# Kernel optimization log

Hardware: AMD Instinct MI355X
Metric: run time of the kernel (lower is better)

## Reference

```python
import jax, jax.numpy as jnp
import numpy as np

N = 100000
E = 1600000
D = 64
ED = 16
L = 3


def setup_inputs() -> dict:
    key = jax.random.key(0)
    ks = jax.random.split(key, 12)
    s = 1.0 / np.sqrt(D)
    se = 1.0 / np.sqrt(ED)
    return {
        "x": jax.random.normal(ks[0], (N, D), dtype=jnp.float32),
        "edge_index": jax.random.randint(ks[1], (2, E), 0, N, dtype=jnp.int64),
        "edge_attr": jax.random.normal(ks[2], (E, ED), dtype=jnp.float32),
        "Wk": jax.random.normal(ks[3], (L, D, D), dtype=jnp.float32) * s,
        "bk": jnp.zeros((L, D), dtype=jnp.float32),
        "Wq": jax.random.normal(ks[4], (L, D, D), dtype=jnp.float32) * s,
        "bq": jnp.zeros((L, D), dtype=jnp.float32),
        "Wv": jax.random.normal(ks[5], (L, D, D), dtype=jnp.float32) * s,
        "bv": jnp.zeros((L, D), dtype=jnp.float32),
        "We": jax.random.normal(ks[6], (L, ED, D), dtype=jnp.float32) * se,
        "be": jnp.zeros((L, D), dtype=jnp.float32),
        "Wskip": jax.random.normal(ks[7], (L, D, D), dtype=jnp.float32) * s,
        "bias": jnp.zeros((L, D), dtype=jnp.float32),
        "Wl": jax.random.normal(ks[8], (D, 1), dtype=jnp.float32) * s,
        "bl": jnp.zeros((1,), dtype=jnp.float32),
    }


def _res_gated_conv(h, src, dst, edge_attr, Wk, bk, Wq, bq, Wv, bv, We, be, Wskip, bias):
    # PyG ResGatedGraphConv: eta = sigmoid(k_i + q_j + lin_edge(e)); out_i = sum_j eta * v_j + lin_skip(x_i) + bias
    k = h @ Wk + bk            # [N, D]
    q = h @ Wq + bq            # [N, D]
    v = h @ Wv + bv            # [N, D]
    e = edge_attr @ We + be    # [E, D]
    gate = jax.nn.sigmoid(k[dst] + q[src] + e)   # [E, D]
    msg = gate * v[src]                          # [E, D]
    agg = jax.ops.segment_sum(msg, dst, num_segments=N)  # scatter-add to targets
    return agg + h @ Wskip + bias


def reference(x, edge_index, edge_attr, Wk, bk, Wq, bq, Wv, bv, We, be, Wskip, bias, Wl, bl):
    src = edge_index[0]  # j (source, flow source_to_target)
    dst = edge_index[1]  # i (target)
    h = x
    h = jax.nn.elu(_res_gated_conv(h, src, dst, edge_attr, Wk[0], bk[0], Wq[0], bq[0], Wv[0], bv[0], We[0], be[0], Wskip[0], bias[0]))
    feat = jax.nn.elu(_res_gated_conv(h, src, dst, edge_attr, Wk[1], bk[1], Wq[1], bq[1], Wv[1], bv[1], We[1], be[1], Wskip[1], bias[1]))
    h = jax.nn.elu(_res_gated_conv(feat, src, dst, edge_attr, Wk[2], bk[2], Wq[2], bq[2], Wv[2], bv[2], We[2], be[2], Wskip[2], bias[2]))
    logits = h @ Wl + bl                         # [N, 1]
    return (jax.nn.sigmoid(logits), feat, jnp.concatenate((feat, logits), axis=1))
```

## Files before the change

### kernel.cpp

```cpp
#include <hip/hip_runtime.h>
#include <hip/hip_bf16.h>
#include <math.h>


#define D_CH 64
#define E_CH 16

__device__ __forceinline__ float bcastf(float v, int srclane) {
  return __int_as_float(__builtin_amdgcn_readlane(__float_as_int(v), srclane));
}

__global__ void k_detect(const unsigned int* __restrict__ ei, int* __restrict__ flag,
                         int n_samples) {
  __shared__ unsigned int red[256];
  unsigned int acc = 0;
  for (int i = threadIdx.x; i < n_samples; i += 256) acc |= ei[2 * i + 1];
  red[threadIdx.x] = acc;
  __syncthreads();
  for (int s = 128; s > 0; s >>= 1) {
    if (threadIdx.x < s) red[threadIdx.x] |= red[threadIdx.x + s];
    __syncthreads();
  }
  if (threadIdx.x == 0) flag[0] = (red[0] == 0u) ? 1 : 0;
}

__global__ void k_normalize(const void* __restrict__ ei, const int* __restrict__ flag,
                            int* __restrict__ src, int* __restrict__ dst, int E) {
  int e = blockIdx.x * blockDim.x + threadIdx.x;
  if (e >= E) return;
  if (flag[0]) {
    const long long* p = (const long long*)ei;
    src[e] = (int)p[e];
    dst[e] = (int)p[E + e];
  } else {
    const int* p = (const int*)ei;
    src[e] = p[e];
    dst[e] = p[E + e];
  }
}

__global__ void k_zero(int* __restrict__ p, int n) {
  int i = blockIdx.x * blockDim.x + threadIdx.x;
  if (i < n) p[i] = 0;
}

__global__ void k_hist(const int* __restrict__ dst, int* __restrict__ deg, int E) {
  int e = blockIdx.x * blockDim.x + threadIdx.x;
  if (e < E) atomicAdd(&deg[dst[e]], 1);
}

__global__ void k_scan(int* __restrict__ deg_cursor, int* __restrict__ offsets, int N) {
  __shared__ int buf[1024];
  __shared__ int carry;
  if (threadIdx.x == 0) carry = 0;
  __syncthreads();
  for (int base = 0; base < N; base += 1024) {
    int i = base + threadIdx.x;
    int val = (i < N) ? deg_cursor[i] : 0;
    buf[threadIdx.x] = val;
    __syncthreads();
    for (int off = 1; off < 1024; off <<= 1) {
      int t = (threadIdx.x >= off) ? buf[threadIdx.x - off] : 0;
      __syncthreads();
      buf[threadIdx.x] += t;
      __syncthreads();
    }
    int excl = buf[threadIdx.x] - val;
    int c = carry;
    int tot = buf[1023];
    __syncthreads();
    if (i < N) {
      offsets[i] = c + excl;
      deg_cursor[i] = c + excl;
    }
    if (threadIdx.x == 0) carry = c + tot;
    __syncthreads();
  }
  if (threadIdx.x == 0) offsets[N] = carry;
}

__global__ void k_scatter(const int* __restrict__ src, const int* __restrict__ dst,
                          int* __restrict__ cursor, int* __restrict__ csr_src,
                          int* __restrict__ csr_eid, int E) {
  int e = blockIdx.x * blockDim.x + threadIdx.x;
  if (e >= E) return;
  int d = dst[e];
  int p = atomicAdd(&cursor[d], 1);
  csr_src[p] = src[e];
  csr_eid[p] = e;
}

__global__ __launch_bounds__(256, 1) void k_nodelin(
    const float* __restrict__ hin, const float* __restrict__ Wa,
    const float* __restrict__ ba, const float* __restrict__ Wb,
    const float* __restrict__ bb, float* __restrict__ outa, float* __restrict__ outb,
    int N) {
  int lane = threadIdx.x & 63;
  int wave = blockIdx.x * (blockDim.x >> 6) + (threadIdx.x >> 6);
  int nwaves = gridDim.x * (blockDim.x >> 6);
  float wa[64], wb[64];
#pragma unroll
  for (int c = 0; c < 64; ++c) {
    wa[c] = Wa[c * 64 + lane];
    wb[c] = Wb[c * 64 + lane];
  }
  float bav = ba[lane], bbv = bb[lane];
  for (int i = wave; i < N; i += nwaves) {
    float h = hin[(size_t)i * 64 + lane];
    float a = bav, b = bbv;
#pragma unroll
    for (int c = 0; c < 64; ++c) {
      float hc = bcastf(h, c);
      a = fmaf(hc, wa[c], a);
      b = fmaf(hc, wb[c], b);
    }
    outa[(size_t)i * 64 + lane] = a;
    outb[(size_t)i * 64 + lane] = b;
  }
}

template <int MODE>
__global__ __launch_bounds__(256, 4) void k_edge(
    const int* __restrict__ offsets, const int* __restrict__ csr_src,
    const int* __restrict__ csr_eid, const float* __restrict__ kk,
    const float* __restrict__ qq, const float* __restrict__ vv,
    const float* __restrict__ base, const float* __restrict__ ea,
    const float* __restrict__ We, const float* __restrict__ be,
    float* __restrict__ hnext, float* __restrict__ dout,
    const float* __restrict__ Wl, const float* __restrict__ bl, int N) {
  int lane = threadIdx.x & 63;
  int wave = blockIdx.x * (blockDim.x >> 6) + (threadIdx.x >> 6);
  int nwaves = gridDim.x * (blockDim.x >> 6);
  float we[16];
#pragma unroll
  for (int c = 0; c < 16; ++c) we[c] = We[c * 64 + lane];
  float bev = be[lane];
  float wl = (MODE == 2) ? Wl[lane] : 0.f;
  float bl0 = (MODE == 2) ? bl[0] : 0.f;
  for (int i = wave; i < N; i += nwaves) {
    float ki = kk[(size_t)i * 64 + lane] + bev;
    float acc = base[(size_t)i * 64 + lane];
    int p0 = __builtin_amdgcn_readfirstlane(offsets[i]);
    int p1 = __builtin_amdgcn_readfirstlane(offsets[i + 1]);
    for (int p = p0; p < p1; ++p) {
      int j = __builtin_amdgcn_readfirstlane(csr_src[p]);
      int eid = __builtin_amdgcn_readfirstlane(csr_eid[p]);
      const float4* eaq = (const float4*)(ea + (size_t)eid * E_CH);
      float4 e0 = eaq[0], e1 = eaq[1], e2 = eaq[2], e3 = eaq[3];
      float ev = 0.f;
      ev = fmaf(e0.x, we[0], ev);  ev = fmaf(e0.y, we[1], ev);
      ev = fmaf(e0.z, we[2], ev);  ev = fmaf(e0.w, we[3], ev);
      ev = fmaf(e1.x, we[4], ev);  ev = fmaf(e1.y, we[5], ev);
      ev = fmaf(e1.z, we[6], ev);  ev = fmaf(e1.w, we[7], ev);
      ev = fmaf(e2.x, we[8], ev);  ev = fmaf(e2.y, we[9], ev);
      ev = fmaf(e2.z, we[10], ev); ev = fmaf(e2.w, we[11], ev);
      ev = fmaf(e3.x, we[12], ev); ev = fmaf(e3.y, we[13], ev);
      ev = fmaf(e3.z, we[14], ev); ev = fmaf(e3.w, we[15], ev);
      float qj = qq[(size_t)j * 64 + lane];
      float vj = vv[(size_t)j * 64 + lane];
      float g = ki + qj + ev;
      g = 1.0f / (1.0f + __expf(-g));
      acc = fmaf(g, vj, acc);
    }
    float r = (acc > 0.f) ? acc : expm1f(acc);
    if (MODE == 0) {
      hnext[(size_t)i * 64 + lane] = r;
    } else if (MODE == 1) {
      hnext[(size_t)i * 64 + lane] = r;
      dout[(size_t)N + (size_t)i * 64 + lane] = r;
      dout[(size_t)N * 65 + (size_t)i * 65 + lane] = r;
    } else {
      float dot = r * wl;
#pragma unroll
      for (int m = 32; m >= 1; m >>= 1) dot += __shfl_xor(dot, m);
      float logit = dot + bl0;
      if (lane == 0) {
        dout[i] = 1.0f / (1.0f + __expf(-logit));
        dout[(size_t)N * 65 + (size_t)i * 65 + 64] = logit;
      }
    }
  }
}

extern "C" void kernel_launch(void* const* d_in, const int* in_sizes, int n_in,
                              void* d_out, int out_size, void* d_ws, size_t ws_size,
                              hipStream_t stream) {
  const float* x   = (const float*)d_in[0];
  const void*  ei  = d_in[1];
  const float* ea  = (const float*)d_in[2];
  const float* Wk  = (const float*)d_in[3];
  const float* bk  = (const float*)d_in[4];
  const float* Wq  = (const float*)d_in[5];
  const float* bq  = (const float*)d_in[6];
  const float* Wv  = (const float*)d_in[7];
  const float* bv  = (const float*)d_in[8];
  const float* We  = (const float*)d_in[9];
  const float* be  = (const float*)d_in[10];
  const float* Ws  = (const float*)d_in[11];
  const float* bia = (const float*)d_in[12];
  const float* Wl  = (const float*)d_in[13];
  const float* bl  = (const float*)d_in[14];
  int N = in_sizes[0] / D_CH;
  int E = in_sizes[2] / E_CH;

  char* w = (char*)d_ws;
  auto alloc = [&](size_t bytes) -> char* {
    char* r = w;
    w += (bytes + 255) & ~(size_t)255;
    return r;
  };
  int* flag     = (int*)alloc(16);
  int* src      = (int*)alloc((size_t)E * 4);
  int* dstA     = (int*)alloc((size_t)E * 4);
  int* offsets  = (int*)alloc((size_t)(N + 1) * 4);
  int* cursor   = (int*)alloc((size_t)N * 4);
  int* csr_src  = (int*)alloc((size_t)E * 4);
  int* csr_eid  = (int*)alloc((size_t)E * 4);
  float* kk     = (float*)alloc((size_t)N * D_CH * 4);
  float* qqb    = (float*)alloc((size_t)N * D_CH * 4);
  float* vvb    = (float*)alloc((size_t)N * D_CH * 4);
  float* baseb  = (float*)alloc((size_t)N * D_CH * 4);
  float* h1     = (float*)alloc((size_t)N * D_CH * 4);
  float* feat   = (float*)alloc((size_t)N * D_CH * 4);
  float* dout   = (float*)d_out;

  int gE = (E + 255) / 256;
  int gN = (N + 255) / 256;

  k_detect<<<1, 256, 0, stream>>>((const unsigned int*)ei, flag, 8192);
  k_normalize<<<gE, 256, 0, stream>>>(ei, flag, src, dstA, E);
  k_zero<<<gN, 256, 0, stream>>>(cursor, N);
  k_hist<<<gE, 256, 0, stream>>>(dstA, cursor, E);
  k_scan<<<1, 1024, 0, stream>>>(cursor, offsets, N);
  k_scatter<<<gE, 256, 0, stream>>>(src, dstA, cursor, csr_src, csr_eid, E);

  const float* hin = x;
  for (int l = 0; l < 3; ++l) {
    const float* Wk_l = Wk + (size_t)l * 4096;
    const float* bk_l = bk + (size_t)l * 64;
    const float* Wq_l = Wq + (size_t)l * 4096;
    const float* bq_l = bq + (size_t)l * 64;
    const float* Wv_l = Wv + (size_t)l * 4096;
    const float* bv_l = bv + (size_t)l * 64;
    const float* We_l = We + (size_t)l * 1024;
    const float* be_l = be + (size_t)l * 64;
    const float* Ws_l = Ws + (size_t)l * 4096;
    const float* bi_l = bia + (size_t)l * 64;

    k_nodelin<<<1024, 256, 0, stream>>>(hin, Wk_l, bk_l, Wq_l, bq_l, kk, qqb, N);
    k_nodelin<<<1024, 256, 0, stream>>>(hin, Wv_l, bv_l, Ws_l, bi_l, vvb, baseb, N);
    if (l == 0) {
      k_edge<0><<<2048, 256, 0, stream>>>(offsets, csr_src, csr_eid, kk, qqb, vvb,
                                          baseb, ea, We_l, be_l, h1, dout, Wl, bl, N);
      hin = h1;
    } else if (l == 1) {
      k_edge<1><<<2048, 256, 0, stream>>>(offsets, csr_src, csr_eid, kk, qqb, vvb,
                                          baseb, ea, We_l, be_l, feat, dout, Wl, bl, N);
      hin = feat;
    } else {
      k_edge<2><<<2048, 256, 0, stream>>>(offsets, csr_src, csr_eid, kk, qqb, vvb,
                                          baseb, ea, We_l, be_l, h1, dout, Wl, bl, N);
    }
  }
}
```

Baseline: 1.524 ms.

## Batch edge metadata loads, interleave q/v rows, and parallelize CSR build scan

The edge kernel now loads up to 64 packed (src, eid) pairs per wave in one coalesced load, broadcasts them with readlane, and unrolls four edges so their gathers are in flight together. This replaces the serialized per-edge scalar metadata loads. The q and v projections are written interleaved per node so one source row covers both gathers. The CSR build fuses normalize with the histogram, replaces the single-block scan with a three-kernel parallel scan, and packs csr_src and csr_eid into int2. The unroll raises register pressure, so launch bounds drop from 4 to 3 blocks per CU.

```diff
diff --git a/kernel.cpp b/kernel.cpp
--- a/kernel.cpp
+++ b/kernel.cpp
@@ -6,95 +6,148 @@
 #define D_CH 64
 #define E_CH 16
 
+__global__ void k_prep(const unsigned int* __restrict__ ei, int* __restrict__ flag,
+                       int* __restrict__ deg, int N, int nsamp) {
+  int i = blockIdx.x * blockDim.x + threadIdx.x;
+  if (i < N) deg[i] = 0;
+  if (blockIdx.x == 0) {
+    unsigned int acc = 0;
+    for (int s = threadIdx.x; s < nsamp; s += blockDim.x) acc |= ei[2 * s + 1];
+    int nz = __syncthreads_or(acc != 0u);
+    if (threadIdx.x == 0) flag[0] = nz ? 0 : 1;
+  }
+}
+
+__global__ void k_normhist(const void* __restrict__ ei, const int* __restrict__ flag,
+                           int* __restrict__ src, int* __restrict__ dstA,
+                           int* __restrict__ deg, int E) {
+  int e = blockIdx.x * blockDim.x + threadIdx.x;
+  if (e >= E) return;
+  int s, d;
+  if (flag[0]) {
+    const long long* p = (const long long*)ei;
+    s = (int)p[e];
+    d = (int)p[E + e];
+  } else {
+    const int* p = (const int*)ei;
+    s = p[e];
+    d = p[E + e];
+  }
+  src[e] = s;
+  dstA[e] = d;
+  atomicAdd(&deg[d], 1);
+}
+
+__global__ void k_scanpart(const int* __restrict__ deg, int* __restrict__ partial, int N) {
+  __shared__ int wsum[4];
+  int tid = threadIdx.x, lane = tid & 63, w = tid >> 6;
+  int i0 = blockIdx.x * 1024 + tid * 4;
+  int4 v = make_int4(0, 0, 0, 0);
+  if (i0 + 3 < N) {
+    v = *(const int4*)(deg + i0);
+  } else {
+    if (i0 < N) v.x = deg[i0];
+    if (i0 + 1 < N) v.y = deg[i0 + 1];
+    if (i0 + 2 < N) v.z = deg[i0 + 2];
+  }
+  int s = v.x + v.y + v.z + v.w;
+#pragma unroll
+  for (int m = 32; m; m >>= 1) s += __shfl_xor(s, m);
+  if (lane == 0) wsum[w] = s;
+  __syncthreads();
+  if (tid == 0) partial[blockIdx.x] = wsum[0] + wsum[1] + wsum[2] + wsum[3];
+}
+
+__global__ void k_scanroot(int* __restrict__ partial, int* __restrict__ offsets,
+                           int NB, int N) {
+  if (NB <= 128) {
+    int lane = threadIdx.x;
+    int a = (lane < NB) ? partial[lane] : 0;
+    int b = (lane + 64 < NB) ? partial[lane + 64] : 0;
+    int sa = a, sb = b;
+#pragma unroll
+    for (int off = 1; off < 64; off <<= 1) {
+      int t = __shfl_up(sa, off);
+      if (lane >= off) sa += t;
+      int u = __shfl_up(sb, off);
+      if (lane >= off) sb += u;
+    }
+    int atot = __shfl(sa, 63);
+    sb += atot;
+    int tot = __shfl(sb, 63);
+    if (lane < NB) partial[lane] = sa - a;
+    if (lane + 64 < NB) partial[lane + 64] = sb - b;
+    if (lane == 0) offsets[N] = tot;
+  } else {
+    if (threadIdx.x == 0) {
+      int run = 0;
+      for (int bI = 0; bI < NB; ++bI) {
+        int vv = partial[bI];
+        partial[bI] = run;
+        run += vv;
+      }
+      offsets[N] = run;
+    }
+  }
+}
+
+__global__ void k_scanapply(const int* __restrict__ deg, const int* __restrict__ partial,
+                            int* __restrict__ offsets, int* __restrict__ cursor, int N) {
+  __shared__ int wsum[4];
+  int tid = threadIdx.x, lane = tid & 63, w = tid >> 6;
+  int i0 = blockIdx.x * 1024 + tid * 4;
+  int4 v = make_int4(0, 0, 0, 0);
+  if (i0 + 3 < N) {
+    v = *(const int4*)(deg + i0);
+  } else {
+    if (i0 < N) v.x = deg[i0];
+    if (i0 + 1 < N) v.y = deg[i0 + 1];
+    if (i0 + 2 < N) v.z = deg[i0 + 2];
+  }
+  int ts = v.x + v.y + v.z + v.w;
+  int s = ts;
+#pragma unroll
+  for (int off = 1; off < 64; off <<= 1) {
+    int t = __shfl_up(s, off);
+    if (lane >= off) s += t;
+  }
+  if (lane == 63) wsum[w] = s;
+  __syncthreads();
+  int wb = 0;
+#pragma unroll
+  for (int x = 0; x < 4; ++x)
+    if (x < w) wb += wsum[x];
+  int excl = s - ts + wb + partial[blockIdx.x];
+  int o0 = excl, o1 = o0 + v.x, o2 = o1 + v.y, o3 = o2 + v.z;
+  if (i0 + 3 < N) {
+    int4 o = make_int4(o0, o1, o2, o3);
+    *(int4*)(offsets + i0) = o;
+    *(int4*)(cursor + i0) = o;
+  } else {
+    if (i0 < N) { offsets[i0] = o0; cursor[i0] = o0; }
+    if (i0 + 1 < N) { offsets[i0 + 1] = o1; cursor[i0 + 1] = o1; }
+    if (i0 + 2 < N) { offsets[i0 + 2] = o2; cursor[i0 + 2] = o2; }
+  }
+}
+
+__global__ void k_scatter(const int* __restrict__ src, const int* __restrict__ dstA,
+                          int* __restrict__ cursor, int2* __restrict__ je, int E) {
+  int e = blockIdx.x * blockDim.x + threadIdx.x;
+  if (e >= E) return;
+  int d = dstA[e];
+  int p = atomicAdd(&cursor[d], 1);
+  je[p] = make_int2(src[e], e);
+}
+
 __device__ __forceinline__ float bcastf(float v, int srclane) {
   return __int_as_float(__builtin_amdgcn_readlane(__float_as_int(v), srclane));
-}
-
-__global__ void k_detect(const unsigned int* __restrict__ ei, int* __restrict__ flag,
-                         int n_samples) {
-  __shared__ unsigned int red[256];
-  unsigned int acc = 0;
-  for (int i = threadIdx.x; i < n_samples; i += 256) acc |= ei[2 * i + 1];
-  red[threadIdx.x] = acc;
-  __syncthreads();
-  for (int s = 128; s > 0; s >>= 1) {
-    if (threadIdx.x < s) red[threadIdx.x] |= red[threadIdx.x + s];
-    __syncthreads();
-  }
-  if (threadIdx.x == 0) flag[0] = (red[0] == 0u) ? 1 : 0;
-}
-
-__global__ void k_normalize(const void* __restrict__ ei, const int* __restrict__ flag,
-                            int* __restrict__ src, int* __restrict__ dst, int E) {
-  int e = blockIdx.x * blockDim.x + threadIdx.x;
-  if (e >= E) return;
-  if (flag[0]) {
-    const long long* p = (const long long*)ei;
-    src[e] = (int)p[e];
-    dst[e] = (int)p[E + e];
-  } else {
-    const int* p = (const int*)ei;
-    src[e] = p[e];
-    dst[e] = p[E + e];
-  }
-}
-
-__global__ void k_zero(int* __restrict__ p, int n) {
-  int i = blockIdx.x * blockDim.x + threadIdx.x;
-  if (i < n) p[i] = 0;
-}
-
-__global__ void k_hist(const int* __restrict__ dst, int* __restrict__ deg, int E) {
-  int e = blockIdx.x * blockDim.x + threadIdx.x;
-  if (e < E) atomicAdd(&deg[dst[e]], 1);
-}
-
-__global__ void k_scan(int* __restrict__ deg_cursor, int* __restrict__ offsets, int N) {
-  __shared__ int buf[1024];
-  __shared__ int carry;
-  if (threadIdx.x == 0) carry = 0;
-  __syncthreads();
-  for (int base = 0; base < N; base += 1024) {
-    int i = base + threadIdx.x;
-    int val = (i < N) ? deg_cursor[i] : 0;
-    buf[threadIdx.x] = val;
-    __syncthreads();
-    for (int off = 1; off < 1024; off <<= 1) {
-      int t = (threadIdx.x >= off) ? buf[threadIdx.x - off] : 0;
-      __syncthreads();
-      buf[threadIdx.x] += t;
-      __syncthreads();
-    }
-    int excl = buf[threadIdx.x] - val;
-    int c = carry;
-    int tot = buf[1023];
-    __syncthreads();
-    if (i < N) {
-      offsets[i] = c + excl;
-      deg_cursor[i] = c + excl;
-    }
-    if (threadIdx.x == 0) carry = c + tot;
-    __syncthreads();
-  }
-  if (threadIdx.x == 0) offsets[N] = carry;
-}
-
-__global__ void k_scatter(const int* __restrict__ src, const int* __restrict__ dst,
-                          int* __restrict__ cursor, int* __restrict__ csr_src,
-                          int* __restrict__ csr_eid, int E) {
-  int e = blockIdx.x * blockDim.x + threadIdx.x;
-  if (e >= E) return;
-  int d = dst[e];
-  int p = atomicAdd(&cursor[d], 1);
-  csr_src[p] = src[e];
-  csr_eid[p] = e;
 }
 
 __global__ __launch_bounds__(256, 1) void k_nodelin(
     const float* __restrict__ hin, const float* __restrict__ Wa,
     const float* __restrict__ ba, const float* __restrict__ Wb,
     const float* __restrict__ bb, float* __restrict__ outa, float* __restrict__ outb,
-    int N) {
+    int ostride, int N) {
   int lane = threadIdx.x & 63;
   int wave = blockIdx.x * (blockDim.x >> 6) + (threadIdx.x >> 6);
   int nwaves = gridDim.x * (blockDim.x >> 6);
@@ -114,16 +167,48 @@
       a = fmaf(hc, wa[c], a);
       b = fmaf(hc, wb[c], b);
     }
-    outa[(size_t)i * 64 + lane] = a;
-    outb[(size_t)i * 64 + lane] = b;
-  }
-}
+    outa[(size_t)i * ostride + lane] = a;
+    outb[(size_t)i * ostride + lane] = b;
+  }
+}
+
+#define EDGE_LOAD(K, T)                                                        \
+  int j##K = __builtin_amdgcn_readlane(meta.x, (T));                           \
+  int eI##K = __builtin_amdgcn_readlane(meta.y, (T));                          \
+  const float4* ap##K = (const float4*)(ea + (size_t)eI##K * E_CH);            \
+  float4 eA##K##a = ap##K[0], eA##K##b = ap##K[1], eA##K##c = ap##K[2],        \
+         eA##K##d = ap##K[3];                                                  \
+  float q##K = qv[(size_t)j##K * 128 + lane];                                  \
+  float v##K = qv[(size_t)j##K * 128 + 64 + lane];
+
+#define EDGE_COMP(K)                                                           \
+  {                                                                            \
+    float ev = 0.f;                                                            \
+    ev = fmaf(eA##K##a.x, we[0], ev);                                          \
+    ev = fmaf(eA##K##a.y, we[1], ev);                                          \
+    ev = fmaf(eA##K##a.z, we[2], ev);                                          \
+    ev = fmaf(eA##K##a.w, we[3], ev);                                          \
+    ev = fmaf(eA##K##b.x, we[4], ev);                                          \
+    ev = fmaf(eA##K##b.y, we[5], ev);                                          \
+    ev = fmaf(eA##K##b.z, we[6], ev);                                          \
+    ev = fmaf(eA##K##b.w, we[7], ev);                                          \
+    ev = fmaf(eA##K##c.x, we[8], ev);                                          \
+    ev = fmaf(eA##K##c.y, we[9], ev);                                          \
+    ev = fmaf(eA##K##c.z, we[10], ev);                                         \
+    ev = fmaf(eA##K##c.w, we[11], ev);                                         \
+    ev = fmaf(eA##K##d.x, we[12], ev);                                         \
+    ev = fmaf(eA##K##d.y, we[13], ev);                                         \
+    ev = fmaf(eA##K##d.z, we[14], ev);                                         \
+    ev = fmaf(eA##K##d.w, we[15], ev);                                         \
+    float g = ki + q##K + ev;                                                  \
+    g = 1.0f / (1.0f + __expf(-g));                                            \
+    acc = fmaf(g, v##K, acc);                                                  \
+  }
 
 template <int MODE>
-__global__ __launch_bounds__(256, 4) void k_edge(
-    const int* __restrict__ offsets, const int* __restrict__ csr_src,
-    const int* __restrict__ csr_eid, const float* __restrict__ kk,
-    const float* __restrict__ qq, const float* __restrict__ vv,
+__global__ __launch_bounds__(256, 3) void k_edge(
+    const int* __restrict__ offsets, const int2* __restrict__ je,
+    const float* __restrict__ kk, const float* __restrict__ qv,
     const float* __restrict__ base, const float* __restrict__ ea,
     const float* __restrict__ We, const float* __restrict__ be,
     float* __restrict__ hnext, float* __restrict__ dout,
@@ -142,25 +227,26 @@
     float acc = base[(size_t)i * 64 + lane];
     int p0 = __builtin_amdgcn_readfirstlane(offsets[i]);
     int p1 = __builtin_amdgcn_readfirstlane(offsets[i + 1]);
-    for (int p = p0; p < p1; ++p) {
-      int j = __builtin_amdgcn_readfirstlane(csr_src[p]);
-      int eid = __builtin_amdgcn_readfirstlane(csr_eid[p]);
-      const float4* eaq = (const float4*)(ea + (size_t)eid * E_CH);
-      float4 e0 = eaq[0], e1 = eaq[1], e2 = eaq[2], e3 = eaq[3];
-      float ev = 0.f;
-      ev = fmaf(e0.x, we[0], ev);  ev = fmaf(e0.y, we[1], ev);
-      ev = fmaf(e0.z, we[2], ev);  ev = fmaf(e0.w, we[3], ev);
-      ev = fmaf(e1.x, we[4], ev);  ev = fmaf(e1.y, we[5], ev);
-      ev = fmaf(e1.z, we[6], ev);  ev = fmaf(e1.w, we[7], ev);
-      ev = fmaf(e2.x, we[8], ev);  ev = fmaf(e2.y, we[9], ev);
-      ev = fmaf(e2.z, we[10], ev); ev = fmaf(e2.w, we[11], ev);
-      ev = fmaf(e3.x, we[12], ev); ev = fmaf(e3.y, we[13], ev);
-      ev = fmaf(e3.z, we[14], ev); ev = fmaf(e3.w, we[15], ev);
-      float qj = qq[(size_t)j * 64 + lane];
-      float vj = vv[(size_t)j * 64 + lane];
-      float g = ki + qj + ev;
-      g = 1.0f / (1.0f + __expf(-g));
-      acc = fmaf(g, vj, acc);
+    for (int pb = p0; pb < p1; pb += 64) {
+      int m = p1 - pb;
+      if (m > 64) m = 64;
+      int idx = pb + ((lane < m) ? lane : 0);
+      int2 meta = je[idx];
+      int t = 0;
+      for (; t + 4 <= m; t += 4) {
+        EDGE_LOAD(0, t)
+        EDGE_LOAD(1, t + 1)
+        EDGE_LOAD(2, t + 2)
+        EDGE_LOAD(3, t + 3)
+        EDGE_COMP(0)
+        EDGE_COMP(1)
+        EDGE_COMP(2)
+        EDGE_COMP(3)
+      }
+      for (; t < m; ++t) {
+        EDGE_LOAD(5, t)
+        EDGE_COMP(5)
+      }
     }
     float r = (acc > 0.f) ? acc : expm1f(acc);
     if (MODE == 0) {
@@ -172,7 +258,7 @@
     } else {
       float dot = r * wl;
 #pragma unroll
-      for (int m = 32; m >= 1; m >>= 1) dot += __shfl_xor(dot, m);
+      for (int m2 = 32; m2 >= 1; m2 >>= 1) dot += __shfl_xor(dot, m2);
       float logit = dot + bl0;
       if (lane == 0) {
         dout[i] = 1.0f / (1.0f + __expf(-logit));
@@ -202,6 +288,7 @@
   const float* bl  = (const float*)d_in[14];
   int N = in_sizes[0] / D_CH;
   int E = in_sizes[2] / E_CH;
+  int NB = (N + 1023) / 1024;
 
   char* w = (char*)d_ws;
   auto alloc = [&](size_t bytes) -> char* {
@@ -212,13 +299,13 @@
   int* flag     = (int*)alloc(16);
   int* src      = (int*)alloc((size_t)E * 4);
   int* dstA     = (int*)alloc((size_t)E * 4);
+  int* deg      = (int*)alloc((size_t)N * 4);
+  int* partial  = (int*)alloc((size_t)NB * 4);
   int* offsets  = (int*)alloc((size_t)(N + 1) * 4);
   int* cursor   = (int*)alloc((size_t)N * 4);
-  int* csr_src  = (int*)alloc((size_t)E * 4);
-  int* csr_eid  = (int*)alloc((size_t)E * 4);
+  int2* je      = (int2*)alloc((size_t)E * 8);
   float* kk     = (float*)alloc((size_t)N * D_CH * 4);
-  float* qqb    = (float*)alloc((size_t)N * D_CH * 4);
-  float* vvb    = (float*)alloc((size_t)N * D_CH * 4);
+  float* qv     = (float*)alloc((size_t)N * 128 * 4);
   float* baseb  = (float*)alloc((size_t)N * D_CH * 4);
   float* h1     = (float*)alloc((size_t)N * D_CH * 4);
   float* feat   = (float*)alloc((size_t)N * D_CH * 4);
@@ -227,12 +314,12 @@
   int gE = (E + 255) / 256;
   int gN = (N + 255) / 256;
 
-  k_detect<<<1, 256, 0, stream>>>((const unsigned int*)ei, flag, 8192);
-  k_normalize<<<gE, 256, 0, stream>>>(ei, flag, src, dstA, E);
-  k_zero<<<gN, 256, 0, stream>>>(cursor, N);
-  k_hist<<<gE, 256, 0, stream>>>(dstA, cursor, E);
-  k_scan<<<1, 1024, 0, stream>>>(cursor, offsets, N);
-  k_scatter<<<gE, 256, 0, stream>>>(src, dstA, cursor, csr_src, csr_eid, E);
+  k_prep<<<gN, 256, 0, stream>>>((const unsigned int*)ei, flag, deg, N, 8192);
+  k_normhist<<<gE, 256, 0, stream>>>(ei, flag, src, dstA, deg, E);
+  k_scanpart<<<NB, 256, 0, stream>>>(deg, partial, N);
+  k_scanroot<<<1, 64, 0, stream>>>(partial, offsets, NB, N);
+  k_scanapply<<<NB, 256, 0, stream>>>(deg, partial, offsets, cursor, N);
+  k_scatter<<<gE, 256, 0, stream>>>(src, dstA, cursor, je, E);
 
   const float* hin = x;
   for (int l = 0; l < 3; ++l) {
@@ -247,19 +334,19 @@
     const float* Ws_l = Ws + (size_t)l * 4096;
     const float* bi_l = bia + (size_t)l * 64;
 
-    k_nodelin<<<1024, 256, 0, stream>>>(hin, Wk_l, bk_l, Wq_l, bq_l, kk, qqb, N);
-    k_nodelin<<<1024, 256, 0, stream>>>(hin, Wv_l, bv_l, Ws_l, bi_l, vvb, baseb, N);
+    k_nodelin<<<1024, 256, 0, stream>>>(hin, Wk_l, bk_l, Ws_l, bi_l, kk, baseb, 64, N);
+    k_nodelin<<<1024, 256, 0, stream>>>(hin, Wq_l, bq_l, Wv_l, bv_l, qv, qv + 64, 128, N);
     if (l == 0) {
-      k_edge<0><<<2048, 256, 0, stream>>>(offsets, csr_src, csr_eid, kk, qqb, vvb,
-                                          baseb, ea, We_l, be_l, h1, dout, Wl, bl, N);
+      k_edge<0><<<2048, 256, 0, stream>>>(offsets, je, kk, qv, baseb, ea, We_l, be_l,
+                                          h1, dout, Wl, bl, N);
       hin = h1;
     } else if (l == 1) {
-      k_edge<1><<<2048, 256, 0, stream>>>(offsets, csr_src, csr_eid, kk, qqb, vvb,
-                                          baseb, ea, We_l, be_l, feat, dout, Wl, bl, N);
+      k_edge<1><<<2048, 256, 0, stream>>>(offsets, je, kk, qv, baseb, ea, We_l, be_l,
+                                          feat, dout, Wl, bl, N);
       hin = feat;
     } else {
-      k_edge<2><<<2048, 256, 0, stream>>>(offsets, csr_src, csr_eid, kk, qqb, vvb,
-                                          baseb, ea, We_l, be_l, h1, dout, Wl, bl, N);
-    }
-  }
-}
+      k_edge<2><<<2048, 256, 0, stream>>>(offsets, je, kk, qv, baseb, ea, We_l, be_l,
+                                          h1, dout, Wl, bl, N);
+    }
+  }
+}
```

Measured after the change: 1.270 ms. -16.7%, faster.
